# Optimization experiments

Hardware: AMD Instinct MI355X
Metric: run time of the kernel (lower is better)

Reference implementation:

```python
import jax, jax.numpy as jnp
import numpy as np
import math

PHI = (1.0 + math.sqrt(5.0)) / 2.0
ALPHA = 0.01
I_ROT = math.pi / 2.0
B, IN, H = 4096, 1024, 1024
GIN = IN + 4 * H  # input + 2H (h flat) + 2H (surfaced flat)


def _mag(z):
    return jnp.sqrt(z[..., 0] ** 2 + z[..., 1] ** 2 + 1e-8)


def _phase(z):
    return jnp.arctan2(z[..., 1], z[..., 0] + 1e-10)


@jax.custom_vjp
def fractal_compress(mag):
    m = jnp.maximum(mag, 1e-8)
    return m ** (2.0 / 3.0)


def _fc_fwd(mag):
    m = jnp.maximum(mag, 1e-8)
    c = m ** (2.0 / 3.0)
    return c, c / (m + 1e-6)


def _fc_bwd(ratio, g):
    return (g * jnp.minimum(ratio, 2.0),)


fractal_compress.defvjp(_fc_fwd, _fc_bwd)


def converge(z):
    mag = _mag(z)
    ph = _phase(z)
    cm = fractal_compress(mag)
    return jnp.stack([cm * jnp.cos(ph), cm * jnp.sin(ph)], axis=-1)


def resonance_gate(a, b):
    d = _phase(a) - _phase(b)
    return jnp.cos(d / 2.0) ** 2


def _uni(k, shape, fan_in):
    s = (1.0 / PHI) / math.sqrt(fan_in)
    return jax.random.uniform(k, shape, jnp.float32, -s, s)


def setup_inputs() -> dict:
    key = jax.random.key(0)
    ks = jax.random.split(key, 12)
    return {
        "x_t": jax.random.normal(ks[0], (B, IN), jnp.float32),
        "h_prev": jax.random.normal(ks[1], (B, H, 2), jnp.float32),
        "c_prev": jax.random.normal(ks[2], (B, H, 2), jnp.float32),
        "d_prev": jax.random.normal(ks[3], (B, H, 2), jnp.float32),
        "b_prev": jax.random.uniform(ks[4], (B, 1), jnp.float32),
        "Wf_w": _uni(ks[5], (H, GIN), GIN), "Wf_b": jnp.zeros((H,), jnp.float32),
        "Wi_w": _uni(ks[6], (H, GIN), GIN), "Wi_b": jnp.zeros((H,), jnp.float32),
        "Wo_w": _uni(ks[7], (H, GIN), GIN), "Wo_b": jnp.zeros((H,), jnp.float32),
        "Wc_w": _uni(ks[8], (2 * H, GIN), GIN), "Wc_b": jnp.zeros((2 * H,), jnp.float32),
        "Wr_w": _uni(ks[9], (2 * H, IN), IN), "Wr_b": jnp.zeros((2 * H,), jnp.float32),
        "theta": jnp.full((H,), I_ROT, jnp.float32),
    }


def reference(x_t, h_prev, c_prev, d_prev, b_prev,
              Wf_w, Wf_b, Wi_w, Wi_b, Wo_w, Wo_b, Wc_w, Wc_b, Wr_w, Wr_b, theta):
    batch = x_t.shape[0]
    hid = theta.shape[0]

    # boundary: real input -> complex
    x_complex = (x_t @ Wr_w.T + Wr_b).reshape(batch, hid, 2)

    # memory surfacing from the (detached) worldline
    d_read = jax.lax.stop_gradient(d_prev)
    T = resonance_gate(x_complex, d_read)                      # (B, H)
    d_mag = _mag(d_read)[..., None]                            # (B, H, 1)
    d_normed = d_read / (d_mag + 1e-8)
    d_scale = jnp.sqrt(jnp.clip(d_mag, 1e-6, 20.0))
    surfaced = d_normed * d_scale * T[..., None]               # (B, H, 2)

    combined = jnp.concatenate(
        [x_t, h_prev.reshape(batch, -1), surfaced.reshape(batch, -1)], axis=-1)

    f_raw = combined @ Wf_w.T + Wf_b
    i_raw = combined @ Wi_w.T + Wi_b
    o_raw = combined @ Wo_w.T + Wo_b

    temperature = (2.0 * b_prev + 1e-4)[..., None]             # (B, 1, 1)
    gate_stack = jnp.stack([f_raw, i_raw, o_raw], axis=-1)     # (B, H, 3)
    gw = jax.nn.softmax(gate_stack / temperature, axis=-1)
    f_t, i_t, o_t = gw[..., 0], gw[..., 1], gw[..., 2]

    g_raw = combined @ Wc_w.T + Wc_b
    g_t = jnp.stack([jnp.tanh(g_raw[:, :hid]), jnp.tanh(g_raw[:, hid:])], axis=-1)

    # convergence: released surface -> fractal-compressed -> worldline
    released = (1.0 - f_t)[..., None] * c_prev
    compressed = jnp.clip(converge(released), -10.0, 10.0)
    d_t = jax.lax.stop_gradient(d_prev) + ALPHA * compressed
    d_mag_new = _mag(d_t)[..., None]
    d_t = jnp.where(d_mag_new > 20.0, d_t * (20.0 / d_mag_new), d_t)

    # cell update + i-rotation
    c_updated = f_t[..., None] * c_prev + i_t[..., None] * g_t
    cos_t = jnp.cos(theta)[None, :, None]
    sin_t = jnp.sin(theta)[None, :, None]
    cr, ci = c_updated[..., 0:1], c_updated[..., 1:2]
    c_t = jnp.concatenate([cos_t * cr - sin_t * ci, sin_t * cr + cos_t * ci], axis=-1)

    c_squashed = jnp.stack([jnp.tanh(c_t[..., 0]), jnp.tanh(c_t[..., 1])], axis=-1)
    h_raw = o_t[..., None] * c_squashed
    G = resonance_gate(h_raw, d_t)
    h_t = G[..., None] * h_raw

    # balance update from energy split
    conv_e = (_mag(released) ** 2).sum(axis=-1, keepdims=True)
    emer_e = (_mag(h_t) ** 2).sum(axis=-1, keepdims=True)
    b_measured = conv_e / (conv_e + emer_e + 1e-8)
    b_t = 0.99 * b_prev + 0.01 * b_measured

    h_t = jnp.nan_to_num(h_t, nan=0.0)
    c_t = jnp.nan_to_num(c_t, nan=0.0)
    d_t = jnp.nan_to_num(d_t, nan=0.0)
    b_t = jnp.nan_to_num(b_t, nan=0.5)
    return (h_t, c_t, d_t, b_t)
```

## Files before the change

### kernel.cpp

```cpp
#include <hip/hip_runtime.h>
#include <math.h>

typedef unsigned short u16;
typedef unsigned int u32;
typedef u16 u16x4 __attribute__((ext_vector_type(4)));
typedef float f32x2 __attribute__((ext_vector_type(2)));
typedef float f32x4 __attribute__((ext_vector_type(4)));
typedef __bf16 bf16x8 __attribute__((ext_vector_type(8)));

#define CAPF 256

__device__ __forceinline__ u16 f2bf(float f){
  u32 u = __builtin_bit_cast(u32, f);
  u32 r = u + 0x7FFFu + ((u >> 16) & 1u);
  return (u16)(r >> 16);
}
__device__ __forceinline__ float bf2f(u16 h){
  u32 u = ((u32)h) << 16;
  return __builtin_bit_cast(float, u);
}
__device__ __forceinline__ float ftanh(float x){
  float e = __expf(2.f*x);
  return 1.f - 2.f/(e+1.f);
}

typedef __attribute__((address_space(1))) const unsigned int gas_u32;
typedef __attribute__((address_space(3))) unsigned int las_u32;
__device__ __forceinline__ void gload_lds16(const void* g, void* l){
  __builtin_amdgcn_global_load_lds((gas_u32*)g, (las_u32*)l, 16, 0, 0);
}

__global__ __launch_bounds__(256) void prep0(
    const float* __restrict__ x, const float* __restrict__ h,
    u16* __restrict__ cA, u16* __restrict__ xlo,
    const float* __restrict__ Wr, u16* __restrict__ Wr_hi, u16* __restrict__ Wr_lo,
    const float* __restrict__ bp, int* __restrict__ idx, int* __restrict__ smap,
    float* __restrict__ rawfix)
{
  const int bx = blockIdx.x, tid = threadIdx.x;
  if (bx < 12288){
    int b = bx / 3, cb = bx - b*3;
    int c0 = (cb*256 + tid)*4;
    f32x4 v;
    if (c0 < 1024) v = *(const f32x4*)(x + (size_t)b*1024 + c0);
    else           v = *(const f32x4*)(h + (size_t)b*2048 + (c0-1024));
    u16x4 hi4;
    #pragma unroll
    for (int j=0;j<4;++j) hi4[j]=f2bf(v[j]);
    *(u16x4*)(cA + (size_t)b*5120 + c0) = hi4;
    if (c0 < 1024){
      u16x4 lo4;
      #pragma unroll
      for (int j=0;j<4;++j) lo4[j]=f2bf(v[j]-bf2f(hi4[j]));
      *(u16x4*)(xlo + (size_t)b*1024 + c0) = lo4;
    }
  } else if (bx < 14336){
    int i = (bx-12288)*256 + tid;
    f32x4 v = *(const f32x4*)(Wr + (size_t)i*4);
    u16x4 oh, ol;
    #pragma unroll
    for (int j=0;j<4;++j){ u16 hh=f2bf(v[j]); oh[j]=hh; ol[j]=f2bf(v[j]-bf2f(hh)); }
    *(u16x4*)(Wr_hi + (size_t)i*4) = oh;
    *(u16x4*)(Wr_lo + (size_t)i*4) = ol;
  } else if (bx < 15104){
    int i = (bx-14336)*256 + tid;
    *(f32x4*)(rawfix + (size_t)i*4) = f32x4{0.f,0.f,0.f,0.f};
  } else {
    __shared__ int cnt;
    if (tid==0) cnt=0;
    __syncthreads();
    for (int i=tid; i<4096; i+=256){
      int p = -1;
      if (bp[i] < 0.04f){
        p = atomicAdd(&cnt,1);
        if (p < CAPF) idx[1+p]=i;
      }
      smap[i] = p;
    }
    __syncthreads();
    if (tid==0) idx[0] = min(cnt, CAPF);
  }
}

__global__ __launch_bounds__(256) void cvtW3(
    const float* __restrict__ W0, const float* __restrict__ W1, const float* __restrict__ W2,
    u16* __restrict__ out)
{
  int i = blockIdx.x*256 + threadIdx.x;
  int seg = i / 1310720;
  int w = i - seg*1310720;
  const float* src = (seg==0) ? W0 : (seg==1 ? W1 : W2);
  f32x4 v = *(const f32x4*)(src + (size_t)w*4);
  u16x4 o;
  #pragma unroll
  for (int j=0;j<4;++j) o[j]=f2bf(v[j]);
  *(u16x4*)(out + (size_t)seg*5242880 + (size_t)w*4) = o;
}

__global__ __launch_bounds__(256) void cvt_hi(const float* __restrict__ in, u16* __restrict__ out, int n4){
  int i = blockIdx.x*256 + threadIdx.x;
  if (i >= n4) return;
  f32x4 v = *(const f32x4*)(in + (size_t)i*4);
  u16x4 o;
  #pragma unroll
  for (int j=0;j<4;++j) o[j]=f2bf(v[j]);
  *(u16x4*)(out + (size_t)i*4) = o;
}

__global__ __launch_bounds__(256) void prep_surf(const float* __restrict__ xc, const float* __restrict__ dp,
                                                 const int* __restrict__ smap, float* __restrict__ Scmp,
                                                 u16* __restrict__ cA){
  int i = blockIdx.x*256 + threadIdx.x;
  int b = i >> 10, h = i & 1023;
  f32x2 z = *(const f32x2*)(xc + 2*(size_t)i);
  f32x2 d = *(const f32x2*)(dp + 2*(size_t)i);
  float zx = z[0] + 1e-10f, dx = d[0] + 1e-10f;
  float hz = sqrtf(zx*zx + z[1]*z[1]);
  float hd = sqrtf(dx*dx + d[1]*d[1]);
  float cosd = (zx*dx + z[1]*d[1]) / fmaxf(hz*hd, 1e-30f);
  float T = 0.5f + 0.5f*cosd;
  float dmag = sqrtf(d[0]*d[0] + d[1]*d[1] + 1e-8f);
  float dscale = sqrtf(fminf(fmaxf(dmag, 1e-6f), 20.0f));
  float s = T * dscale / (dmag + 1e-8f);
  float o0 = d[0]*s, o1 = d[1]*s;
  u32 pk = (u32)f2bf(o0) | ((u32)f2bf(o1) << 16);
  *(u32*)&cA[(size_t)b*5120 + 3072 + 2*h] = pk;
  int p = smap[b];
  if (p >= 0 && p < CAPF)
    *(f32x2*)(Scmp + ((size_t)p*1024 + h)*2) = f32x2{o0, o1};
}

#define LDA8(BUF,H,MH,J) (*(const bf16x8*)(sAc + ((BUF)*2+(H))*16384 + abase + (MH)*4096 + (J)*1024))
#define LDB8(BUF,H,N)    (*(const bf16x8*)(sBc + ((BUF)*2+(H))*16384 + bbase + (N)*1024))
#define STG_A8(BUF,H,TT) { const u16* s_ = Ah + aS + (size_t)(TT)*64 + (H)*32; \
    gload_lds16(s_, dA + ((BUF)*2+(H))*8192); \
    gload_lds16(s_ + aS2, dA + ((BUF)*2+(H))*8192 + 4096); }
#define STG_B8(BUF,H,TT) { const u16* s_ = Bh + bS + (size_t)(TT)*64 + (H)*32; \
    gload_lds16(s_, dB + ((BUF)*2+(H))*8192); \
    gload_lds16(s_ + bS2, dB + ((BUF)*2+(H))*8192 + 4096); }
#define PH8(BUF,H,MH,RB,STG,DOW) do{ \
    bf16x8 af0 = LDA8(BUF,H,MH,0), af1 = LDA8(BUF,H,MH,1), af2 = LDA8(BUF,H,MH,2), af3 = LDA8(BUF,H,MH,3); \
    if (RB){ _Pragma("unroll") for(int n_=0;n_<NR;++n_) bfr[n_] = LDB8(BUF,H,n_); } \
    STG; \
    asm volatile("" ::: "memory"); \
    __builtin_amdgcn_s_barrier(); \
    __builtin_amdgcn_s_setprio(1); \
    _Pragma("unroll") for(int n_=0;n_<NR;++n_){ \
      acc[(MH)*4+0][n_] = __builtin_amdgcn_mfma_f32_16x16x32_bf16(af0, bfr[n_], acc[(MH)*4+0][n_],0,0,0); \
      acc[(MH)*4+1][n_] = __builtin_amdgcn_mfma_f32_16x16x32_bf16(af1, bfr[n_], acc[(MH)*4+1][n_],0,0,0); \
      acc[(MH)*4+2][n_] = __builtin_amdgcn_mfma_f32_16x16x32_bf16(af2, bfr[n_], acc[(MH)*4+2][n_],0,0,0); \
      acc[(MH)*4+3][n_] = __builtin_amdgcn_mfma_f32_16x16x32_bf16(af3, bfr[n_], acc[(MH)*4+3][n_],0,0,0); } \
    __builtin_amdgcn_s_setprio(0); \
    if (DOW) { asm volatile("s_waitcnt vmcnt(%0)" :: "i"(VN) : "memory"); } \
    asm volatile("" ::: "memory"); \
    __builtin_amdgcn_s_barrier(); \
  }while(0)

template<int NR, bool OUTBF, int NB>
__global__ __launch_bounds__(512) void gemm8p(
    const u16* __restrict__ Ah, int lda,
    const u16* __restrict__ Bh, int ldb,
    const float* __restrict__ bias0, const float* __restrict__ bias1, const float* __restrict__ bias2,
    float* __restrict__ Cf, u16* __restrict__ Cb, int ldc, int K)
{
  constexpr int BN   = NR*64;
  constexpr int VN   = 8;
  __shared__ u16 sA[4*8192];
  __shared__ u16 sB[4*8192];
  const char* sAc = (const char*)sA;
  const char* sBc = (const char*)sB;

  const int tid = threadIdx.x, lane = tid&63, w8 = tid>>6;
  const int wr = w8>>2, wc = w8&3;
  const int l16 = lane&15;

  const int gx = gridDim.x, nwg = gx*gridDim.y;
  const int lin = blockIdx.y*gx + blockIdx.x;
  const int sw = (lin&7)*(nwg>>3) + (lin>>3);
  const int m0 = (sw / gx)*256, n0 = (sw % gx)*BN;

  const int rowS  = tid>>2;
  const int ksS   = (tid&3) ^ ((tid>>3)&3);
  const size_t aS = (size_t)(m0 + rowS)*lda + ksS*8;
  const size_t aS2= (size_t)128*lda;
  const size_t bS = (size_t)(n0 + rowS)*ldb + ksS*8;
  const size_t bS2= (size_t)128*ldb;
  u16* dA = sA + w8*512;
  u16* dB = sB + w8*512;

  const int aslot = (lane>>4) ^ ((l16>>1)&3);
  const int abase = (wr*128 + l16)*64 + aslot*16;
  const int bbase = (wc*(NR*16) + l16)*64 + aslot*16;

  f32x4 acc[8][NR];
  #pragma unroll
  for (int a=0;a<8;++a)
    #pragma unroll
    for (int b=0;b<NR;++b) acc[a][b] = f32x4{0.f,0.f,0.f,0.f};
  bf16x8 bfr[NR];

  const int NT = K>>6, NITER = K>>7;

  STG_A8(0,0,0) STG_B8(0,0,0) STG_A8(0,1,0) STG_B8(0,1,0) STG_A8(1,0,1) STG_B8(1,0,1)
  asm volatile("s_waitcnt vmcnt(%0)" :: "i"(VN) : "memory");
  asm volatile("" ::: "memory");
  __builtin_amdgcn_s_barrier();

  for (int i=0; i<NITER; ++i){
    const int t1 = 2*i+1;
    const int ta = min(2*i+2, NT-1);
    const int tb = min(2*i+3, NT-1);
    PH8(0,0,0,true,  STG_A8(1,1,t1), false);
    PH8(0,0,1,false, STG_B8(1,1,t1), true);
    PH8(0,1,0,true,  STG_A8(0,0,ta), false);
    PH8(0,1,1,false, STG_B8(0,0,ta), true);
    PH8(1,0,0,true,  STG_A8(0,1,ta), false);
    PH8(1,0,1,false, STG_B8(0,1,ta), true);
    PH8(1,1,0,true,  STG_A8(1,0,tb), false);
    PH8(1,1,1,false, STG_B8(1,0,tb), true);
  }
  asm volatile("s_waitcnt vmcnt(0)" ::: "memory");

  #pragma unroll
  for (int mf=0; mf<8; ++mf){
    int grow = m0 + wr*128 + mf*16 + (lane>>4)*4;
    #pragma unroll
    for (int n=0; n<NR; ++n){
      int gcol = n0 + wc*(NR*16) + n*16 + l16;
      float bb;
      if constexpr(NB==3) bb = (gcol<1024) ? bias0[gcol] : ((gcol<2048) ? bias1[gcol-1024] : bias2[gcol-2048]);
      else bb = bias0[gcol];
      #pragma unroll
      for (int r2=0;r2<4;++r2){
        float v = acc[mf][n][r2] + bb;
        if constexpr(OUTBF) Cb[(size_t)(grow+r2)*ldc + gcol] = f2bf(v);
        else                Cf[(size_t)(grow+r2)*ldc + gcol] = v;
      }
    }
  }
}

#define STG128(USRC, BW) do{ int u_=(USRC)<NT?(USRC):NT-1; \
    { const u16* s_=Ah+aS+(size_t)u_*32; gload_lds16(s_, sA+(BW)*4096+ldsb); } \
    { const u16* s_=Bh+bS+(size_t)u_*32; gload_lds16(s_, sB+(BW)*8192+ldsb); \
      gload_lds16(s_+bS2, sB+(BW)*8192+4096+ldsb); } \
    if constexpr(SPLIT){ \
      const u16* s2_=Al+aSl+(size_t)u_*32; gload_lds16(s2_, sAl+(BW)*4096+ldsb); \
      const u16* s3_=Bl+bS+(size_t)u_*32;  gload_lds16(s3_, sBl+(BW)*8192+ldsb); \
      gload_lds16(s3_+bS2, sBl+(BW)*8192+4096+ldsb); } \
  }while(0)

template<bool SPLIT, bool OUTBF, int BUFS>
__global__ __launch_bounds__(512) void gemm128(
    const u16* __restrict__ Ah, int lda,
    const u16* __restrict__ Al, int ldal,
    const u16* __restrict__ Bh, int ldb,
    const u16* __restrict__ Bl,
    const float* __restrict__ bias0,
    float* __restrict__ Cf, u16* __restrict__ Cb, int ldc, int K)
{
  constexpr int LPS = SPLIT ? 6 : 3;
  constexpr int VN  = (BUFS-2)*LPS;
  constexpr int PRE = BUFS-1;
  __shared__ u16 sA [BUFS*4096];
  __shared__ u16 sB [BUFS*8192];
  __shared__ u16 sAl[SPLIT?BUFS*4096:8];
  __shared__ u16 sBl[SPLIT?BUFS*8192:8];

  const int tid=threadIdx.x, lane=tid&63, w8=tid>>6;
  const int wr=w8>>2, wc=w8&3, l16=lane&15;

  const int gx=gridDim.x, nwg=gx*gridDim.y;
  const int lin=blockIdx.y*gx+blockIdx.x;
  const int sw=(lin&7)*(nwg>>3)+(lin>>3);
  const int m0=(sw/gx)*128, n0=(sw%gx)*256;

  const int rowS=tid>>2;
  const int ksS=(tid&3)^((tid>>3)&3);
  const size_t aS =(size_t)(m0+rowS)*lda  + ksS*8;
  const size_t aSl=(size_t)(m0+rowS)*(size_t)ldal + ksS*8;
  const size_t bS =(size_t)(n0+rowS)*ldb  + ksS*8;
  const size_t bS2=(size_t)128*ldb;
  const int ldsb = w8*512;

  const int aslot=(lane>>4)^((l16>>1)&3);
  const int abase=(wr*64+l16)*64 + aslot*16;
  const int bbase=(wc*64+l16)*64 + aslot*16;

  f32x4 acc[4][4];
  #pragma unroll
  for (int a=0;a<4;++a)
    #pragma unroll
    for (int b=0;b<4;++b) acc[a][b] = f32x4{0.f,0.f,0.f,0.f};

  const int NT = K>>5;

  #pragma unroll
  for (int u=0; u<PRE; ++u){ STG128(u,u); }
  asm volatile("s_waitcnt vmcnt(%0)" :: "i"(VN) : "memory");
  asm volatile("" ::: "memory");
  __builtin_amdgcn_s_barrier();

  int bufR = 0;
  for (int t=0; t<NT; ++t){
    int bufW = (bufR==0) ? BUFS-1 : bufR-1;
    const char* sAc=(const char*)sA  + bufR*8192;
    const char* sBc=(const char*)sB  + bufR*16384;
    const char* sAlc=(const char*)sAl + bufR*8192;
    const char* sBlc=(const char*)sBl + bufR*16384;
    bf16x8 af[4], bf[4], afl[4], bfl[4];
    #pragma unroll
    for (int f=0; f<4; ++f){
      af[f] = *(const bf16x8*)(sAc + abase + f*1024);
      bf[f] = *(const bf16x8*)(sBc + bbase + f*1024);
      if constexpr(SPLIT){
        afl[f] = *(const bf16x8*)(sAlc + abase + f*1024);
        bfl[f] = *(const bf16x8*)(sBlc + bbase + f*1024);
      }
    }
    STG128(t+PRE, bufW);
    asm volatile("" ::: "memory");
    __builtin_amdgcn_s_barrier();
    __builtin_amdgcn_s_setprio(1);
    #pragma unroll
    for (int mf=0; mf<4; ++mf){
      #pragma unroll
      for (int nf=0; nf<4; ++nf){
        acc[mf][nf] = __builtin_amdgcn_mfma_f32_16x16x32_bf16(af[mf], bf[nf], acc[mf][nf],0,0,0);
        if constexpr(SPLIT){
          acc[mf][nf] = __builtin_amdgcn_mfma_f32_16x16x32_bf16(afl[mf], bf[nf],  acc[mf][nf],0,0,0);
          acc[mf][nf] = __builtin_amdgcn_mfma_f32_16x16x32_bf16(af[mf],  bfl[nf], acc[mf][nf],0,0,0);
        }
      }
    }
    __builtin_amdgcn_s_setprio(0);
    asm volatile("s_waitcnt vmcnt(%0)" :: "i"(VN) : "memory");
    asm volatile("" ::: "memory");
    __builtin_amdgcn_s_barrier();
    bufR = (bufR+1==BUFS) ? 0 : bufR+1;
  }
  asm volatile("s_waitcnt vmcnt(0)" ::: "memory");

  #pragma unroll
  for (int mf=0; mf<4; ++mf){
    int grow = m0 + wr*64 + mf*16 + (lane>>4)*4;
    #pragma unroll
    for (int nf=0; nf<4; ++nf){
      int gcol = n0 + wc*64 + nf*16 + l16;
      float bb = bias0[gcol];
      #pragma unroll
      for (int r2=0;r2<4;++r2){
        float v = acc[mf][nf][r2] + bb;
        if constexpr(OUTBF) Cb[(size_t)(grow+r2)*ldc + gcol] = f2bf(v);
        else                Cf[(size_t)(grow+r2)*ldc + gcol] = v;
      }
    }
  }
}

#define LSTR 40
#define FIX_KC 16
#define FIX_KLEN 320
__global__ __launch_bounds__(256) void gemm_fix_sk(
    const float* __restrict__ Xs, const float* __restrict__ Hs,
    const float* __restrict__ Scmp, const int* __restrict__ smap,
    const float* __restrict__ W0, const float* __restrict__ W1, const float* __restrict__ W2,
    const int* __restrict__ cr, float* __restrict__ Cfix)
{
  const int count = cr[0];
  const int m0 = blockIdx.y * 128;
  if (m0 >= count) return;
  const int* rows = cr + 1;
  const int kbeg = blockIdx.z * FIX_KLEN;
  const int kend = kbeg + FIX_KLEN;

  __shared__ u16 sAh[128*LSTR];
  __shared__ u16 sAl[128*LSTR];
  __shared__ u16 sBh[128*LSTR];
  __shared__ u16 sBl[128*LSTR];

  const int tid = threadIdx.x;
  const int n0 = blockIdx.x * 128;
  int seg = n0 >> 10;
  const float* W = (seg==0) ? W0 : (seg==1 ? W1 : W2);
  int nw = n0 & 1023;

  const int wave = tid >> 6, lane = tid & 63;
  const int wm = wave >> 1, wn = wave & 1;
  const int l16 = lane & 15, lk8 = (lane >> 4) * 8;

  f32x4 acc[4][4];
  #pragma unroll
  for (int a=0;a<4;++a)
    #pragma unroll
    for (int b=0;b<4;++b) acc[a][b] = f32x4{0.f,0.f,0.f,0.f};

  for (int k0 = kbeg; k0 < kend; k0 += 32){
    #pragma unroll
    for (int i=0;i<4;++i){
      int flat = tid + i*256;
      int r  = flat >> 3;
      int c4 = flat & 7;
      int kk = k0 + c4*4;
      int mi = min(m0 + r, count-1);
      int mrow = rows[mi];
      const float* srcA;
      if (kk < 1024)      srcA = Xs + (size_t)mrow*1024 + kk;
      else if (kk < 3072) srcA = Hs + (size_t)mrow*2048 + (kk - 1024);
      else                srcA = Scmp + (size_t)smap[mrow]*2048 + (kk - 3072);
      f32x4 va = *(const f32x4*)srcA;
      f32x4 vb = *(const f32x4*)(W + (size_t)(nw + r)*5120 + kk);
      u16x4 ah, bh, al, bl;
      #pragma unroll
      for (int j=0;j<4;++j){
        u16 hA = f2bf(va[j]); ah[j] = hA; al[j] = f2bf(va[j] - bf2f(hA));
        u16 hB = f2bf(vb[j]); bh[j] = hB; bl[j] = f2bf(vb[j] - bf2f(hB));
      }
      int o = r*LSTR + c4*4;
      *(u16x4*)&sAh[o] = ah;
      *(u16x4*)&sBh[o] = bh;
      *(u16x4*)&sAl[o] = al;
      *(u16x4*)&sBl[o] = bl;
    }
    __syncthreads();
    bf16x8 fah[4], fbh[4], fal[4], fbl[4];
    #pragma unroll
    for (int f=0; f<4; ++f){
      int ra  = (wm*64 + f*16 + l16)*LSTR + lk8;
      int rb2 = (wn*64 + f*16 + l16)*LSTR + lk8;
      fah[f] = *(const bf16x8*)&sAh[ra];
      fbh[f] = *(const bf16x8*)&sBh[rb2];
      fal[f] = *(const bf16x8*)&sAl[ra];
      fbl[f] = *(const bf16x8*)&sBl[rb2];
    }
    #pragma unroll
    for (int fm=0; fm<4; ++fm){
      #pragma unroll
      for (int fn=0; fn<4; ++fn){
        acc[fm][fn] = __builtin_amdgcn_mfma_f32_16x16x32_bf16(fah[fm], fbh[fn], acc[fm][fn], 0,0,0);
        acc[fm][fn] = __builtin_amdgcn_mfma_f32_16x16x32_bf16(fal[fm], fbh[fn], acc[fm][fn], 0,0,0);
        acc[fm][fn] = __builtin_amdgcn_mfma_f32_16x16x32_bf16(fah[fm], fbl[fn], acc[fm][fn], 0,0,0);
      }
    }
    __syncthreads();
  }

  #pragma unroll
  for (int fm=0; fm<4; ++fm){
    int trow = wm*64 + fm*16 + (lane>>4)*4;
    #pragma unroll
    for (int fn=0; fn<4; ++fn){
      int lcol = wn*64 + fn*16 + l16;
      #pragma unroll
      for (int r2=0;r2<4;++r2){
        int mi = m0 + trow + r2;
        if (mi < count){
          atomicAdd(&Cfix[(size_t)mi*3072 + (n0 + lcol)], acc[fm][fn][r2]);
        }
      }
    }
  }
}

__global__ __launch_bounds__(256) void epilogue(
    const float* __restrict__ rawfio, const u16* __restrict__ rawg,
    const float* __restrict__ rawfix, const int* __restrict__ smap, const int* __restrict__ cr,
    const float* __restrict__ bf0, const float* __restrict__ bf1, const float* __restrict__ bf2,
    const float* __restrict__ c_prev, const float* __restrict__ d_prev,
    const float* __restrict__ b_prev, const float* __restrict__ theta,
    float* __restrict__ out)
{
  const int b = blockIdx.x;
  const int tid = threadIdx.x;
  float* Hout = out;
  float* Cout = out + (size_t)8388608;
  float* Dout = out + (size_t)16777216;
  float* Bout = out + (size_t)25165824;
  const float bp = b_prev[b];
  const float inv_t = 1.0f / (2.0f*bp + 1e-4f);
  float conv_acc = 0.f, emer_acc = 0.f;
  const size_t rb3 = (size_t)b*3072;
  const size_t rg = (size_t)b*2048;
  const int p = smap[b];
  const bool fx = (p >= 0 && p < cr[0]);
  const size_t rfx = (size_t)p*3072;

  #pragma unroll
  for (int j=0;j<4;++j){
    int h = tid + j*256;
    float fr, ir, og;
    if (fx){
      fr = rawfix[rfx + h]        + bf0[h];
      ir = rawfix[rfx + 1024 + h] + bf1[h];
      og = rawfix[rfx + 2048 + h] + bf2[h];
    } else {
      fr = rawfio[rb3 + h];
      ir = rawfio[rb3 + 1024 + h];
      og = rawfio[rb3 + 2048 + h];
    }
    float g0 = bf2f(rawg[rg + h]);
    float g1 = bf2f(rawg[rg + 1024 + h]);

    float mx = fmaxf(fr, fmaxf(ir, og));
    float ef = __expf((fr-mx)*inv_t);
    float ei = __expf((ir-mx)*inv_t);
    float eo = __expf((og-mx)*inv_t);
    float inv_s = 1.0f/(ef+ei+eo);
    float ft = ef*inv_s, it = ei*inv_s, ot = eo*inv_s;

    f32x2 cp = *(const f32x2*)(c_prev + 2*((size_t)b*1024 + h));
    f32x2 dp = *(const f32x2*)(d_prev + 2*((size_t)b*1024 + h));

    float r0 = (1.f-ft)*cp[0], r1 = (1.f-ft)*cp[1];
    float rm2 = r0*r0 + r1*r1;
    conv_acc += rm2 + 1e-8f;
    float rmag = sqrtf(rm2 + 1e-8f);
    float cm = __expf(0.66666667f * __logf(rmag));
    float rx = r0 + 1e-10f;
    float hr = fmaxf(sqrtf(rx*rx + r1*r1), 1e-30f);
    float invhr = cm / hr;
    float comp0 = fminf(fmaxf(rx*invhr, -10.f), 10.f);
    float comp1 = fminf(fmaxf(r1*invhr, -10.f), 10.f);

    float d0 = dp[0] + 0.01f*comp0;
    float d1 = dp[1] + 0.01f*comp1;
    float dmn = sqrtf(d0*d0 + d1*d1 + 1e-8f);
    if (dmn > 20.f){ float sc = 20.f/dmn; d0*=sc; d1*=sc; }

    float gt0 = ftanh(g0), gt1 = ftanh(g1);
    float cu0 = ft*cp[0] + it*gt0;
    float cu1 = ft*cp[1] + it*gt1;
    float th = theta[h];
    float sth, cth;
    __sincosf(th, &sth, &cth);
    float c0 = cth*cu0 - sth*cu1;
    float c1 = sth*cu0 + cth*cu1;
    float cs0 = ftanh(c0), cs1 = ftanh(c1);
    float hr0 = ot*cs0, hr1 = ot*cs1;

    float hx = hr0 + 1e-10f, dx = d0 + 1e-10f;
    float hh = sqrtf(hx*hx + hr1*hr1);
    float hd = sqrtf(dx*dx + d1*d1);
    float cosd = (hx*dx + hr1*d1) / fmaxf(hh*hd, 1e-30f);
    float G = 0.5f + 0.5f*cosd;
    float h0 = G*hr0, h1 = G*hr1;
    emer_acc += h0*h0 + h1*h1 + 1e-8f;

    h0 = (h0==h0)?h0:0.f;  h1 = (h1==h1)?h1:0.f;
    c0 = (c0==c0)?c0:0.f;  c1 = (c1==c1)?c1:0.f;
    d0 = (d0==d0)?d0:0.f;  d1 = (d1==d1)?d1:0.f;

    size_t oi = 2*((size_t)b*1024 + h);
    *(f32x2*)(Hout+oi) = f32x2{h0,h1};
    *(f32x2*)(Cout+oi) = f32x2{c0,c1};
    *(f32x2*)(Dout+oi) = f32x2{d0,d1};
  }

  #pragma unroll
  for (int off=32; off; off>>=1){
    conv_acc += __shfl_down(conv_acc, off);
    emer_acc += __shfl_down(emer_acc, off);
  }
  __shared__ float sred[8];
  int wv = tid>>6, ln = tid&63;
  if (ln==0){ sred[wv]=conv_acc; sred[4+wv]=emer_acc; }
  __syncthreads();
  if (tid==0){
    float cv = sred[0]+sred[1]+sred[2]+sred[3];
    float em = sred[4]+sred[5]+sred[6]+sred[7];
    float bm = cv/(cv+em+1e-8f);
    float bt = 0.99f*bp + 0.01f*bm;
    bt = (bt==bt)?bt:0.5f;
    Bout[b] = bt;
  }
}

extern "C" void kernel_launch(void* const* d_in, const int* in_sizes, int n_in,
                              void* d_out, int out_size, void* d_ws, size_t ws_size,
                              hipStream_t stream)
{
  const float* x_t    = (const float*)d_in[0];
  const float* h_prev = (const float*)d_in[1];
  const float* c_prev = (const float*)d_in[2];
  const float* d_prev = (const float*)d_in[3];
  const float* b_prev = (const float*)d_in[4];
  const float* Wf_w   = (const float*)d_in[5];
  const float* Wf_b   = (const float*)d_in[6];
  const float* Wi_w   = (const float*)d_in[7];
  const float* Wi_b   = (const float*)d_in[8];
  const float* Wo_w   = (const float*)d_in[9];
  const float* Wo_b   = (const float*)d_in[10];
  const float* Wc_w   = (const float*)d_in[11];
  const float* Wc_b   = (const float*)d_in[12];
  const float* Wr_w   = (const float*)d_in[13];
  const float* Wr_b   = (const float*)d_in[14];
  const float* theta  = (const float*)d_in[15];

  char* W = (char*)d_ws;
  float* rawfio = (float*)W;
  float* xc     = (float*)W;
  u16*   Wr_hi  = (u16*)(W + 50331648);
  u16*   Wr_lo  = (u16*)(W + 50331648 + 4194304);
  u16*   x_lo   = (u16*)(W + 50331648 + 8388608);
  u16*   raw_g  = (u16*)(W + 50331648);
  u16*   cA     = (u16*)(W + 67108864);
  u16*   WD     = (u16*)(W + 109051904);
  int*   idx    = (int*)(W + 140509184);
  int*   smap   = (int*)(W + 140509184 + 16388);
  float* Scmp   = (float*)(W + 140546048);
  float* rawfix = (float*)(W + 140546048 + (size_t)CAPF*2048*4);

  dim3 blk(256);

  prep0<<<15105, blk, 0, stream>>>(x_t, h_prev, cA, x_lo, Wr_w, Wr_hi, Wr_lo,
                                   b_prev, idx, smap, rawfix);
  gemm128<true,false,3><<<dim3(8,32), dim3(512), 0, stream>>>(
      cA, 5120, x_lo, 1024, Wr_hi, 1024, Wr_lo,
      Wr_b, xc, nullptr, 2048, 1024);
  prep_surf<<<16384, blk, 0, stream>>>(xc, d_prev, smap, Scmp, cA);
  gemm_fix_sk<<<dim3(24,8,FIX_KC), blk, 0, stream>>>(
      x_t, h_prev, Scmp, smap, Wf_w, Wi_w, Wo_w, idx, rawfix);
  cvtW3<<<15360, blk, 0, stream>>>(Wf_w, Wi_w, Wo_w, WD);
  gemm8p<3,false,3><<<dim3(16,16), dim3(512), 0, stream>>>(
      cA, 5120, WD, 5120, Wf_b, Wi_b, Wo_b, rawfio, nullptr, 3072, 5120);
  cvt_hi<<<10240, blk, 0, stream>>>(Wc_w, WD, 2621440);
  gemm128<false,true,5><<<dim3(8,32), dim3(512), 0, stream>>>(
      cA, 5120, nullptr, 0, WD, 5120, nullptr,
      Wc_b, nullptr, raw_g, 2048, 5120);
  epilogue<<<4096, blk, 0, stream>>>(rawfio, raw_g, rawfix, smap, idx,
                                     Wf_b, Wi_b, Wo_b,
                                     c_prev, d_prev, b_prev, theta, (float*)d_out);
}
```

Measured before the change: 491.9 us.

## Replace 8-phase GEMM with 4-stage K=32 pipelined GEMM, reuse for Wc

Rewrites the fused f/i/o gate GEMM kernel to stage K in 32-wide slices through a 4-deep LDS ring, prefetching three slices ahead. Each of the 8 warps now owns a 64-row by NF*16-column sub-tile in a 4x2 warp grid, replacing 128 rows in a 2x4 grid. The Wc GEMM also moves from the gemm128 kernel to this template with a 128-wide B tile. The aim is a simpler, more uniform load/compute overlap with a barrier every K=32 slice. The cost is twice as many barriers per K, and changed tile shapes that alter occupancy and data reuse.

```diff
diff --git a/kernel.cpp b/kernel.cpp
--- a/kernel.cpp
+++ b/kernel.cpp
@@ -130,48 +130,59 @@
     *(f32x2*)(Scmp + ((size_t)p*1024 + h)*2) = f32x2{o0, o1};
 }
 
-#define LDA8(BUF,H,MH,J) (*(const bf16x8*)(sAc + ((BUF)*2+(H))*16384 + abase + (MH)*4096 + (J)*1024))
-#define LDB8(BUF,H,N)    (*(const bf16x8*)(sBc + ((BUF)*2+(H))*16384 + bbase + (N)*1024))
-#define STG_A8(BUF,H,TT) { const u16* s_ = Ah + aS + (size_t)(TT)*64 + (H)*32; \
-    gload_lds16(s_, dA + ((BUF)*2+(H))*8192); \
-    gload_lds16(s_ + aS2, dA + ((BUF)*2+(H))*8192 + 4096); }
-#define STG_B8(BUF,H,TT) { const u16* s_ = Bh + bS + (size_t)(TT)*64 + (H)*32; \
-    gload_lds16(s_, dB + ((BUF)*2+(H))*8192); \
-    gload_lds16(s_ + bS2, dB + ((BUF)*2+(H))*8192 + 4096); }
-#define PH8(BUF,H,MH,RB,STG,DOW) do{ \
-    bf16x8 af0 = LDA8(BUF,H,MH,0), af1 = LDA8(BUF,H,MH,1), af2 = LDA8(BUF,H,MH,2), af3 = LDA8(BUF,H,MH,3); \
-    if (RB){ _Pragma("unroll") for(int n_=0;n_<NR;++n_) bfr[n_] = LDB8(BUF,H,n_); } \
-    STG; \
+#define STG96(U) do{ int uc_ = min((U), NH-1); \
+    const u16* sa_ = Ah + aS + (size_t)(uc_>>1)*64 + (uc_&1)*32; \
+    u16* da_ = sA + ((U)&3)*8192 + w8*512; \
+    gload_lds16(sa_, da_); \
+    gload_lds16(sa_ + aS2, da_ + 4096); \
+    const u16* sb_ = Bh + bS + (size_t)(uc_>>1)*64 + (uc_&1)*32; \
+    u16* db_ = sB + ((U)&3)*(BSR*32) + w8*512; \
+    gload_lds16(sb_, db_); \
+    if constexpr (BSR==256){ gload_lds16(sb_ + bS2, db_ + 4096); } \
+  }while(0)
+
+#define PH96(HIDX) do{ \
+    const int h_ = (HIDX); \
+    const char* pa_ = sAc + (h_&3)*16384; \
+    const char* pb_ = sBc + (h_&3)*(BSR*64); \
+    bf16x8 af0 = *(const bf16x8*)(pa_ + abase + 0*1024); \
+    bf16x8 af1 = *(const bf16x8*)(pa_ + abase + 1*1024); \
+    bf16x8 af2 = *(const bf16x8*)(pa_ + abase + 2*1024); \
+    bf16x8 af3 = *(const bf16x8*)(pa_ + abase + 3*1024); \
+    bf16x8 bfr[NF]; \
+    _Pragma("unroll") for(int n_=0;n_<NF;++n_) bfr[n_] = *(const bf16x8*)(pb_ + bbase + n_*1024); \
+    STG96(h_+3); \
     asm volatile("" ::: "memory"); \
     __builtin_amdgcn_s_barrier(); \
     __builtin_amdgcn_s_setprio(1); \
-    _Pragma("unroll") for(int n_=0;n_<NR;++n_){ \
-      acc[(MH)*4+0][n_] = __builtin_amdgcn_mfma_f32_16x16x32_bf16(af0, bfr[n_], acc[(MH)*4+0][n_],0,0,0); \
-      acc[(MH)*4+1][n_] = __builtin_amdgcn_mfma_f32_16x16x32_bf16(af1, bfr[n_], acc[(MH)*4+1][n_],0,0,0); \
-      acc[(MH)*4+2][n_] = __builtin_amdgcn_mfma_f32_16x16x32_bf16(af2, bfr[n_], acc[(MH)*4+2][n_],0,0,0); \
-      acc[(MH)*4+3][n_] = __builtin_amdgcn_mfma_f32_16x16x32_bf16(af3, bfr[n_], acc[(MH)*4+3][n_],0,0,0); } \
+    _Pragma("unroll") for(int n_=0;n_<NF;++n_){ \
+      acc[0][n_] = __builtin_amdgcn_mfma_f32_16x16x32_bf16(af0, bfr[n_], acc[0][n_],0,0,0); \
+      acc[1][n_] = __builtin_amdgcn_mfma_f32_16x16x32_bf16(af1, bfr[n_], acc[1][n_],0,0,0); \
+      acc[2][n_] = __builtin_amdgcn_mfma_f32_16x16x32_bf16(af2, bfr[n_], acc[2][n_],0,0,0); \
+      acc[3][n_] = __builtin_amdgcn_mfma_f32_16x16x32_bf16(af3, bfr[n_], acc[3][n_],0,0,0); } \
     __builtin_amdgcn_s_setprio(0); \
-    if (DOW) { asm volatile("s_waitcnt vmcnt(%0)" :: "i"(VN) : "memory"); } \
+    asm volatile("s_waitcnt vmcnt(%0)" :: "i"(VN) : "memory"); \
     asm volatile("" ::: "memory"); \
     __builtin_amdgcn_s_barrier(); \
   }while(0)
 
-template<int NR, bool OUTBF, int NB>
-__global__ __launch_bounds__(512) void gemm8p(
+template<int NF, int BSR, bool OUTBF, int NB>
+__global__ __launch_bounds__(512) void gemm96(
     const u16* __restrict__ Ah, int lda,
     const u16* __restrict__ Bh, int ldb,
     const float* __restrict__ bias0, const float* __restrict__ bias1, const float* __restrict__ bias2,
     float* __restrict__ Cf, u16* __restrict__ Cb, int ldc, int K)
 {
-  constexpr int BN   = NR*64;
-  constexpr int VN   = 8;
+  constexpr int BN  = NF*32;
+  constexpr int LPH = 2 + (BSR>>7);
+  constexpr int VN  = 2*LPH;
   __shared__ u16 sA[4*8192];
-  __shared__ u16 sB[4*8192];
+  __shared__ u16 sB[4*(BSR*32)];
   const char* sAc = (const char*)sA;
   const char* sBc = (const char*)sB;
 
   const int tid = threadIdx.x, lane = tid&63, w8 = tid>>6;
-  const int wr = w8>>2, wc = w8&3;
+  const int wr = w8>>1, wc = w8&1;
   const int l16 = lane&15;
 
   const int gx = gridDim.x, nwg = gx*gridDim.y;
@@ -185,48 +196,38 @@
   const size_t aS2= (size_t)128*lda;
   const size_t bS = (size_t)(n0 + rowS)*ldb + ksS*8;
   const size_t bS2= (size_t)128*ldb;
-  u16* dA = sA + w8*512;
-  u16* dB = sB + w8*512;
-
-  const int aslot = (lane>>4) ^ ((l16>>1)&3);
-  const int abase = (wr*128 + l16)*64 + aslot*16;
-  const int bbase = (wc*(NR*16) + l16)*64 + aslot*16;
-
-  f32x4 acc[8][NR];
-  #pragma unroll
-  for (int a=0;a<8;++a)
-    #pragma unroll
-    for (int b=0;b<NR;++b) acc[a][b] = f32x4{0.f,0.f,0.f,0.f};
-  bf16x8 bfr[NR];
-
-  const int NT = K>>6, NITER = K>>7;
-
-  STG_A8(0,0,0) STG_B8(0,0,0) STG_A8(0,1,0) STG_B8(0,1,0) STG_A8(1,0,1) STG_B8(1,0,1)
+
+  const int slot  = (lane>>4) ^ ((l16>>1)&3);
+  const int abase = (wr*64 + l16)*64 + slot*16;
+  const int bbase = (wc*(NF*16) + l16)*64 + slot*16;
+
+  f32x4 acc[4][NF];
+  #pragma unroll
+  for (int a=0;a<4;++a)
+    #pragma unroll
+    for (int b=0;b<NF;++b) acc[a][b] = f32x4{0.f,0.f,0.f,0.f};
+
+  const int NH = K>>5;
+
+  STG96(0); STG96(1); STG96(2);
   asm volatile("s_waitcnt vmcnt(%0)" :: "i"(VN) : "memory");
   asm volatile("" ::: "memory");
   __builtin_amdgcn_s_barrier();
 
-  for (int i=0; i<NITER; ++i){
-    const int t1 = 2*i+1;
-    const int ta = min(2*i+2, NT-1);
-    const int tb = min(2*i+3, NT-1);
-    PH8(0,0,0,true,  STG_A8(1,1,t1), false);
-    PH8(0,0,1,false, STG_B8(1,1,t1), true);
-    PH8(0,1,0,true,  STG_A8(0,0,ta), false);
-    PH8(0,1,1,false, STG_B8(0,0,ta), true);
-    PH8(1,0,0,true,  STG_A8(0,1,ta), false);
-    PH8(1,0,1,false, STG_B8(0,1,ta), true);
-    PH8(1,1,0,true,  STG_A8(1,0,tb), false);
-    PH8(1,1,1,false, STG_B8(1,0,tb), true);
+  for (int hh=0; hh<NH; hh+=4){
+    PH96(hh+0);
+    PH96(hh+1);
+    PH96(hh+2);
+    PH96(hh+3);
   }
   asm volatile("s_waitcnt vmcnt(0)" ::: "memory");
 
   #pragma unroll
-  for (int mf=0; mf<8; ++mf){
-    int grow = m0 + wr*128 + mf*16 + (lane>>4)*4;
-    #pragma unroll
-    for (int n=0; n<NR; ++n){
-      int gcol = n0 + wc*(NR*16) + n*16 + l16;
+  for (int mf=0; mf<4; ++mf){
+    int grow = m0 + wr*64 + mf*16 + (lane>>4)*4;
+    #pragma unroll
+    for (int n=0; n<NF; ++n){
+      int gcol = n0 + wc*(NF*16) + n*16 + l16;
       float bb;
       if constexpr(NB==3) bb = (gcol<1024) ? bias0[gcol] : ((gcol<2048) ? bias1[gcol-1024] : bias2[gcol-2048]);
       else bb = bias0[gcol];
@@ -621,12 +622,11 @@
   gemm_fix_sk<<<dim3(24,8,FIX_KC), blk, 0, stream>>>(
       x_t, h_prev, Scmp, smap, Wf_w, Wi_w, Wo_w, idx, rawfix);
   cvtW3<<<15360, blk, 0, stream>>>(Wf_w, Wi_w, Wo_w, WD);
-  gemm8p<3,false,3><<<dim3(16,16), dim3(512), 0, stream>>>(
+  gemm96<6,256,false,3><<<dim3(16,16), dim3(512), 0, stream>>>(
       cA, 5120, WD, 5120, Wf_b, Wi_b, Wo_b, rawfio, nullptr, 3072, 5120);
   cvt_hi<<<10240, blk, 0, stream>>>(Wc_w, WD, 2621440);
-  gemm128<false,true,5><<<dim3(8,32), dim3(512), 0, stream>>>(
-      cA, 5120, nullptr, 0, WD, 5120, nullptr,
-      Wc_b, nullptr, raw_g, 2048, 5120);
+  gemm96<4,128,true,1><<<dim3(16,16), dim3(512), 0, stream>>>(
+      cA, 5120, WD, 5120, Wc_b, nullptr, nullptr, nullptr, raw_g, 2048, 5120);
   epilogue<<<4096, blk, 0, stream>>>(rawfio, raw_g, rawfix, smap, idx,
                                      Wf_b, Wi_b, Wo_b,
                                      c_prev, d_prev, b_prev, theta, (float*)d_out);
```

After: 510.7 us. +3.8%, slower.

## Replace the gate GEMMs with a smaller-tile, more-occupant GEMM kernel

Applied to the files above, without the earlier changes.

Adds gemm2b, a 256-thread GEMM with 128xBN tiles (BN=192 or 128), K-steps of 32, a 3-buffer direct-to-LDS pipeline and a swizzled block order. It replaces the 512-thread gemm8p and gemm128 kernels for the f/i/o and candidate projections. The aim is more workgroups per CU and better latency hiding on the two big K=5120 GEMMs. The trade-off is less data reuse per tile and more barriers per unit of work.

```diff
diff --git a/kernel.cpp b/kernel.cpp
--- a/kernel.cpp
+++ b/kernel.cpp
@@ -128,6 +128,114 @@
   int p = smap[b];
   if (p >= 0 && p < CAPF)
     *(f32x2*)(Scmp + ((size_t)p*1024 + h)*2) = f32x2{o0, o1};
+}
+
+#define STG2B(U, BW) do{ int uc_ = min((U), NH-1); \
+    const u16* sa_ = Ah + aS + (size_t)uc_*32; \
+    u16* da_ = sA + (BW)*4096 + w4*512; \
+    gload_lds16(sa_, da_); \
+    gload_lds16(sa_ + (size_t)64*lda, da_ + 2048); \
+    const u16* sb_ = Bh + bS + (size_t)uc_*32; \
+    u16* db_ = sB + (BW)*BUFB + w4*512; \
+    _Pragma("unroll") for (int j_=0;j_<BNC;++j_) \
+      gload_lds16(sb_ + (size_t)(j_*64)*ldb, db_ + j_*2048); \
+  }while(0)
+
+template<int NF, int BUFS, bool OUTBF, int NB>
+__global__ __launch_bounds__(256) void gemm2b(
+    const u16* __restrict__ Ah, int lda,
+    const u16* __restrict__ Bh, int ldb,
+    const float* __restrict__ bias0, const float* __restrict__ bias1, const float* __restrict__ bias2,
+    float* __restrict__ Cf, u16* __restrict__ Cb, int ldc, int K)
+{
+  constexpr int BN   = NF*32;
+  constexpr int BNC  = BN/64;
+  constexpr int LPH  = 2 + BNC;
+  constexpr int VN   = (BUFS-2)*LPH;
+  constexpr int BUFB = BN*32;
+  __shared__ u16 sA[BUFS*4096];
+  __shared__ u16 sB[BUFS*BUFB];
+
+  const int tid = threadIdx.x, lane = tid&63, w4 = tid>>6;
+  const int wm = w4>>1, wn = w4&1;
+  const int l16 = lane&15;
+
+  const int gx = gridDim.x, nwg = gx*gridDim.y;
+  const int lin = blockIdx.y*gx + blockIdx.x;
+  const int sw = (lin&7)*(nwg>>3) + (lin>>3);
+  const int m0 = (sw / gx)*128, n0 = (sw % gx)*BN;
+
+  const int rowS = tid>>2;
+  const int ksS  = (tid&3) ^ ((tid>>3)&3);
+  const size_t aS = (size_t)(m0 + rowS)*lda + ksS*8;
+  const size_t bS = (size_t)(n0 + rowS)*ldb + ksS*8;
+
+  const int slot  = (lane>>4) ^ ((l16>>1)&3);
+  const int abase = (wm*64 + l16)*32 + slot*8;
+  const int bbase = (wn*(NF*16) + l16)*32 + slot*8;
+
+  f32x4 acc[4][NF];
+  #pragma unroll
+  for (int a=0;a<4;++a)
+    #pragma unroll
+    for (int b=0;b<NF;++b) acc[a][b] = f32x4{0.f,0.f,0.f,0.f};
+
+  const int NH = K>>5;
+
+  #pragma unroll
+  for (int u=0; u<BUFS-1; ++u){ STG2B(u, u); }
+  asm volatile("s_waitcnt vmcnt(%0)" :: "i"(VN) : "memory");
+  asm volatile("" ::: "memory");
+  __builtin_amdgcn_s_barrier();
+
+  int bufR = 0;
+  for (int t=0; t<NH; ++t){
+    int bufW = bufR + (BUFS-1); if (bufW >= BUFS) bufW -= BUFS;
+    const u16* pa_ = sA + bufR*4096;
+    const u16* pb_ = sB + bufR*BUFB;
+    bf16x8 af0 = *(const bf16x8*)(pa_ + abase + 0*512);
+    bf16x8 af1 = *(const bf16x8*)(pa_ + abase + 1*512);
+    bf16x8 af2 = *(const bf16x8*)(pa_ + abase + 2*512);
+    bf16x8 af3 = *(const bf16x8*)(pa_ + abase + 3*512);
+    bf16x8 bfr[NF];
+    #pragma unroll
+    for (int n=0;n<NF;++n) bfr[n] = *(const bf16x8*)(pb_ + bbase + n*512);
+    STG2B(t+BUFS-1, bufW);
+    asm volatile("" ::: "memory");
+    __builtin_amdgcn_s_barrier();
+    __builtin_amdgcn_s_setprio(1);
+    #pragma unroll
+    for (int n=0;n<NF;++n){
+      acc[0][n] = __builtin_amdgcn_mfma_f32_16x16x32_bf16(af0, bfr[n], acc[0][n],0,0,0);
+      acc[1][n] = __builtin_amdgcn_mfma_f32_16x16x32_bf16(af1, bfr[n], acc[1][n],0,0,0);
+      acc[2][n] = __builtin_amdgcn_mfma_f32_16x16x32_bf16(af2, bfr[n], acc[2][n],0,0,0);
+      acc[3][n] = __builtin_amdgcn_mfma_f32_16x16x32_bf16(af3, bfr[n], acc[3][n],0,0,0);
+    }
+    __builtin_amdgcn_s_setprio(0);
+    asm volatile("s_waitcnt vmcnt(%0)" :: "i"(VN) : "memory");
+    asm volatile("" ::: "memory");
+    __builtin_amdgcn_s_barrier();
+    bufR = (bufR+1==BUFS) ? 0 : bufR+1;
+  }
+  asm volatile("s_waitcnt vmcnt(0)" ::: "memory");
+
+  #pragma unroll
+  for (int mf=0; mf<4; ++mf){
+    int grow = m0 + wm*64 + mf*16 + (lane>>4)*4;
+    #pragma unroll
+    for (int n=0; n<NF; ++n){
+      int gcol = n0 + wn*(NF*16) + n*16 + l16;
+      float bb;
+      if constexpr(NB==3) bb = (gcol<1024) ? bias0[gcol] : ((gcol<2048) ? bias1[gcol-1024] : bias2[gcol-2048]);
+      else bb = bias0[gcol];
+      #pragma unroll
+      for (int r2=0;r2<4;++r2){
+        float v = acc[mf][n][r2] + bb;
+        if constexpr(OUTBF) Cb[(size_t)(grow+r2)*ldc + gcol] = f2bf(v);
+        else                Cf[(size_t)(grow+r2)*ldc + gcol] = v;
+      }
+    }
+  }
 }
 
 #define LDA8(BUF,H,MH,J) (*(const bf16x8*)(sAc + ((BUF)*2+(H))*16384 + abase + (MH)*4096 + (J)*1024))
@@ -621,12 +729,11 @@
   gemm_fix_sk<<<dim3(24,8,FIX_KC), blk, 0, stream>>>(
       x_t, h_prev, Scmp, smap, Wf_w, Wi_w, Wo_w, idx, rawfix);
   cvtW3<<<15360, blk, 0, stream>>>(Wf_w, Wi_w, Wo_w, WD);
-  gemm8p<3,false,3><<<dim3(16,16), dim3(512), 0, stream>>>(
+  gemm2b<6,3,false,3><<<dim3(16,32), blk, 0, stream>>>(
       cA, 5120, WD, 5120, Wf_b, Wi_b, Wo_b, rawfio, nullptr, 3072, 5120);
   cvt_hi<<<10240, blk, 0, stream>>>(Wc_w, WD, 2621440);
-  gemm128<false,true,5><<<dim3(8,32), dim3(512), 0, stream>>>(
-      cA, 5120, nullptr, 0, WD, 5120, nullptr,
-      Wc_b, nullptr, raw_g, 2048, 5120);
+  gemm2b<4,3,true,1><<<dim3(16,32), blk, 0, stream>>>(
+      cA, 5120, WD, 5120, Wc_b, nullptr, nullptr, nullptr, raw_g, 2048, 5120);
   epilogue<<<4096, blk, 0, stream>>>(rawfio, raw_g, rawfix, smap, idx,
                                      Wf_b, Wi_b, Wo_b,
                                      c_prev, d_prev, b_prev, theta, (float*)d_out);
```

Result: no change. 498.2 us (+1.3%).
